# Kernel optimization log

Hardware: AMD Instinct MI355X
Metric: run time of the kernel (lower is better)

The kernel has to match this reference:

```python
import jax, jax.numpy as jnp
import numpy as np

B, L, D = 2, 2048, 1024
NUM_HEADS = 16
HEAD_DIM = D // NUM_HEADS


def setup_inputs() -> dict:
    key = jax.random.key(0)
    k1, k2 = jax.random.split(key)
    x = jax.random.normal(k1, (B, L, D), dtype=jnp.float32)
    # torch Linear(input_dim, 3*output_dim, bias=False); store as [in, 3*out] for x @ W
    W_qkv = jax.random.normal(k2, (D, 3 * D), dtype=jnp.float32) * (1.0 / np.sqrt(D))
    return {"x": x, "W_qkv": W_qkv}


def reference(x, W_qkv):
    b, l, d = x.shape
    h, hd = NUM_HEADS, HEAD_DIM
    qkv = x @ W_qkv                                  # [B, L, 3*D]
    qkv = qkv.reshape(b, l, 3, h, hd)
    q = jnp.transpose(qkv[:, :, 0], (0, 2, 1, 3))    # [B, H, L, hd]
    k = jnp.transpose(qkv[:, :, 1], (0, 2, 1, 3))
    v = jnp.transpose(qkv[:, :, 2], (0, 2, 1, 3))
    scale = 1.0 / jnp.sqrt(jnp.asarray(hd, dtype=x.dtype))
    scores = jnp.einsum('bhqd,bhkd->bhqk', q, k) * scale   # [B, H, L, L]
    causal = jnp.triu(jnp.ones((l, l), dtype=bool), k=1)   # True above diagonal -> masked
    scores = jnp.where(causal, -jnp.inf, scores)
    attn = jax.nn.softmax(scores, axis=-1)
    # dropout p=0.0 -> identity (eval mode)
    out = jnp.einsum('bhqk,bhkd->bhqd', attn, v)            # [B, H, L, hd]
    out = jnp.transpose(out, (0, 2, 1, 3)).reshape(b, l, h * hd)
    return out
```

## Files before the change

### kernel.cpp

```cpp
#include <hip/hip_runtime.h>
#include <hip/hip_bf16.h>
#include <math.h>

#define NB_L 2048
#define GM 4096
#define GN 3072
#define GK 1024
#define NROWS 65536
#define SCALE_L2E 0.180336880f

typedef float  f4v __attribute__((ext_vector_type(4)));
typedef short  s4v __attribute__((ext_vector_type(4)));
typedef short  s8v __attribute__((ext_vector_type(8)));

#define MFMA_16x16x32(a, b, c) __builtin_amdgcn_mfma_f32_16x16x32_bf16((a), (b), (c), 0, 0, 0)
#define MFMA_16x16x16(a, b, c) __builtin_amdgcn_mfma_f32_16x16x16bf16_1k((a), (b), (c), 0, 0, 0)

static __device__ __forceinline__ unsigned int bfpk(float a, float b) {
    __hip_bfloat162 h = __float22bfloat162_rn(float2{a, b});
    union { __hip_bfloat162 h2; unsigned int u; } cv; cv.h2 = h; return cv.u;
}
static __device__ __forceinline__ unsigned short bf1(float a) {
    union { __hip_bfloat16 h; unsigned short u; } cv; cv.h = __float2bfloat16(a); return cv.u;
}
static __device__ __forceinline__ float bf2f(unsigned short u) {
    union { unsigned int u; float f; } cv; cv.u = ((unsigned int)u) << 16; return cv.f;
}

static __device__ __forceinline__ void gl_lds16(const ushort* g, ushort* l) {
    __builtin_amdgcn_global_load_lds((const __attribute__((address_space(1))) void*)g,
                                     (__attribute__((address_space(3))) void*)l, 16, 0, 0);
}

__global__ __launch_bounds__(256) void conv_fused(
    const float* __restrict__ X, const float* __restrict__ W,
    ushort* __restrict__ Xb, ushort* __restrict__ Wt)
{
    __shared__ __align__(16) ushort T[64][72];
    const int bid = blockIdx.x, t = threadIdx.x;
    if (bid < 2048) {
        const int i = bid * 256 + t;
        const float4 f0 = ((const float4*)X)[2 * i];
        const float4 f1 = ((const float4*)X)[2 * i + 1];
        uint4 u;
        u.x = bfpk(f0.x, f0.y); u.y = bfpk(f0.z, f0.w);
        u.z = bfpk(f1.x, f1.y); u.w = bfpk(f1.z, f1.w);
        ((uint4*)Xb)[i] = u;
    } else {
        const int wb = bid - 2048;
        const int k0 = (wb & 15) * 64, n0 = (wb >> 4) * 64;
        {
            const int kr = t >> 2, nc0 = (t & 3) * 16;
            const float* src = W + (size_t)(k0 + kr) * GN + n0 + nc0;
#pragma unroll
            for (int u = 0; u < 4; ++u) {
                const float4 v = *(const float4*)(src + 4 * u);
                T[nc0 + 4 * u + 0][kr] = bf1(v.x);
                T[nc0 + 4 * u + 1][kr] = bf1(v.y);
                T[nc0 + 4 * u + 2][kr] = bf1(v.z);
                T[nc0 + 4 * u + 3][kr] = bf1(v.w);
            }
        }
        __syncthreads();
        {
            const int nr = t >> 2, kc0 = (t & 3) * 16;
            ushort* dst = Wt + (size_t)(n0 + nr) * GK + k0 + kc0;
            *(s8v*)dst       = *(const s8v*)&T[nr][kc0];
            *(s8v*)(dst + 8) = *(const s8v*)&T[nr][kc0 + 8];
        }
    }
}

__global__ __launch_bounds__(256, 2) void qkv_gemm_bf16(
    const ushort* __restrict__ Xb, const ushort* __restrict__ Wt,
    ushort* __restrict__ Qh, ushort* __restrict__ Kh, ushort* __restrict__ VT)
{
    __shared__ __align__(16) ushort As[2][2][128][32];
    __shared__ __align__(16) ushort Bs[2][2][192][32];

    const int tid = threadIdx.x;
    const int bid = blockIdx.x;

    const int xcd = bid & 7, idx = bid >> 3;
    const int ytile = ((xcd >> 1) << 3) + (idx & 7);
    const int xtile = ((xcd & 1) << 3) + (idx >> 3);
    const int row0 = ytile << 7;
    const int col0 = xtile * 192;

    const int lane = tid & 63, wn = tid >> 6;
    const int lq = lane & 15, quad = lane >> 4;

    const int rS = tid >> 2, pA = tid & 3;
    const int cA = pA ^ ((rS >> 1) & 3);
    const ushort* gA0 = Xb + (size_t)(row0 + rS) * GK + cA * 8;
    const ushort* gB0 = Wt + (size_t)(col0 + rS) * GK + cA * 8;

    const int pq = (quad ^ ((lq >> 1) & 3)) * 8;
    const int rowB = wn * 48;

    f4v acc[8][3];
#pragma unroll
    for (int mf = 0; mf < 8; ++mf)
#pragma unroll
        for (int nf = 0; nf < 3; ++nf) acc[mf][nf] = 0.f;

    auto stA = [&](int t, int h, int u) {
        gl_lds16(gA0 + (size_t)u * 64 * GK + t * 64 + h * 32,
                 &As[t & 1][h][u * 64 + rS][pA * 8]);
    };
    auto stB = [&](int t, int h, int u) {
        gl_lds16(gB0 + (size_t)u * 64 * GK + t * 64 + h * 32,
                 &Bs[t & 1][h][u * 64 + rS][pA * 8]);
    };

    stA(0, 0, 0); stA(0, 0, 1);
    stB(0, 0, 0); stB(0, 0, 1); stB(0, 0, 2);
    stA(0, 1, 0); stA(0, 1, 1);
    stB(0, 1, 0); stB(0, 1, 1); stB(0, 1, 2);
    stA(1, 0, 0); stA(1, 0, 1);
    stB(1, 0, 0); stB(1, 0, 1); stB(1, 0, 2);
    asm volatile("s_waitcnt vmcnt(5)" ::: "memory");
    __builtin_amdgcn_s_barrier();
    asm volatile("" ::: "memory");

    const int NT = GK / 64;
#pragma unroll 2
    for (int t = 0; t < NT; ++t) {
        const int cur = t & 1;
        s8v af[4], bfr[3];

#pragma unroll
        for (int nf = 0; nf < 3; ++nf) bfr[nf] = *(const s8v*)&Bs[cur][0][rowB + nf * 16 + lq][pq];
#pragma unroll
        for (int mf = 0; mf < 4; ++mf) af[mf] = *(const s8v*)&As[cur][0][mf * 16 + lq][pq];
        if (t + 1 < NT) { stB(t + 1, 1, 0); stB(t + 1, 1, 1); stB(t + 1, 1, 2); }
        __builtin_amdgcn_s_barrier();
        asm volatile("s_waitcnt lgkmcnt(0)");
        __builtin_amdgcn_s_setprio(1);
#pragma unroll
        for (int mf = 0; mf < 4; ++mf)
#pragma unroll
            for (int nf = 0; nf < 3; ++nf)
                acc[mf][nf] = MFMA_16x16x32(af[mf], bfr[nf], acc[mf][nf]);
        __builtin_amdgcn_s_setprio(0);
        __builtin_amdgcn_s_barrier();

#pragma unroll
        for (int mf = 0; mf < 4; ++mf) af[mf] = *(const s8v*)&As[cur][0][64 + mf * 16 + lq][pq];
        if (t + 1 < NT) { stA(t + 1, 1, 0); stA(t + 1, 1, 1); }
        __builtin_amdgcn_s_barrier();
        asm volatile("s_waitcnt lgkmcnt(0)");
        __builtin_amdgcn_s_setprio(1);
#pragma unroll
        for (int mf = 0; mf < 4; ++mf)
#pragma unroll
            for (int nf = 0; nf < 3; ++nf)
                acc[mf + 4][nf] = MFMA_16x16x32(af[mf], bfr[nf], acc[mf + 4][nf]);
        __builtin_amdgcn_s_setprio(0);
        __builtin_amdgcn_s_barrier();

#pragma unroll
        for (int nf = 0; nf < 3; ++nf) bfr[nf] = *(const s8v*)&Bs[cur][1][rowB + nf * 16 + lq][pq];
#pragma unroll
        for (int mf = 0; mf < 4; ++mf) af[mf] = *(const s8v*)&As[cur][1][mf * 16 + lq][pq];
        if (t + 2 < NT) { stA(t + 2, 0, 0); stA(t + 2, 0, 1); }
        __builtin_amdgcn_s_barrier();
        asm volatile("s_waitcnt lgkmcnt(0)");
        __builtin_amdgcn_s_setprio(1);
#pragma unroll
        for (int mf = 0; mf < 4; ++mf)
#pragma unroll
            for (int nf = 0; nf < 3; ++nf)
                acc[mf][nf] = MFMA_16x16x32(af[mf], bfr[nf], acc[mf][nf]);
        __builtin_amdgcn_s_setprio(0);
        __builtin_amdgcn_s_barrier();

#pragma unroll
        for (int mf = 0; mf < 4; ++mf) af[mf] = *(const s8v*)&As[cur][1][64 + mf * 16 + lq][pq];
        if (t + 2 < NT) { stB(t + 2, 0, 0); stB(t + 2, 0, 1); stB(t + 2, 0, 2); }
        __builtin_amdgcn_s_barrier();
        asm volatile("s_waitcnt lgkmcnt(0)");
        __builtin_amdgcn_s_setprio(1);
#pragma unroll
        for (int mf = 0; mf < 4; ++mf)
#pragma unroll
            for (int nf = 0; nf < 3; ++nf)
                acc[mf + 4][nf] = MFMA_16x16x32(af[mf], bfr[nf], acc[mf + 4][nf]);
        __builtin_amdgcn_s_setprio(0);
        if (t + 2 < NT) asm volatile("s_waitcnt vmcnt(5)" ::: "memory");
        else            asm volatile("s_waitcnt vmcnt(0)" ::: "memory");
        __builtin_amdgcn_s_barrier();
        asm volatile("" ::: "memory");
    }

#pragma unroll
    for (int mf = 0; mf < 8; ++mf)
#pragma unroll
        for (int nf = 0; nf < 3; ++nf) {
            const int colg = col0 + wn * 48 + nf * 16 + lq;
            const int part = colg >> 10;
            const int colp = colg & 1023;
            const int hh = colp >> 6, d = colp & 63;
#pragma unroll
            for (int r = 0; r < 4; ++r) {
                const int row = row0 + mf * 16 + quad * 4 + r;
                const int b = row >> 11, tok = row & 2047;
                const int bh = b * 16 + hh;
                if (part == 0) {
                    Qh[((size_t)bh * 2048 + tok) * 64 + d] = bf1(acc[mf][nf][r] * SCALE_L2E);
                } else if (part == 1) {
                    Kh[((size_t)bh * 2048 + tok) * 64 + (d ^ ((tok & 7) << 3))] = bf1(acc[mf][nf][r]);
                } else {
                    VT[((size_t)bh * 64 + d) * 2048 + (tok ^ ((d & 7) << 3))] = bf1(acc[mf][nf][r]);
                }
            }
        }
}

__global__ __launch_bounds__(256, 4) void attn_bf16(
    const ushort* __restrict__ Qh, const ushort* __restrict__ Kh,
    const ushort* __restrict__ VT, ushort* __restrict__ Opart, float* __restrict__ Lp)
{
    __shared__ __align__(16) ushort Ks[2][64 * 64];
    __shared__ __align__(16) ushort Vt[2][64 * 64];

    const int x = blockIdx.x;
    const int bh = x & 31;
    const int qlow = (x >> 5) & 7;
    const int s = (x >> 8) & 1;
    const int x9 = (x >> 9) & 1;
    const int qt = x9 ? (15 - qlow) : qlow;

    const int tid = threadIdx.x;
    const int w = tid >> 6, lane = tid & 63;
    const int lq = lane & 15, quad = lane >> 4;
    const int kswz = (lq & 7) << 3;
    const int qrow_base = qt * 128 + w * 32;
    const int diag = 2 * qt + (w >> 1);

    s8v qf[2][2];
#pragma unroll
    for (int qg = 0; qg < 2; ++qg)
#pragma unroll
        for (int sb = 0; sb < 2; ++sb)
            qf[qg][sb] = *(const s8v*)(Qh + ((size_t)bh * 2048 + qrow_base + qg * 16 + lq) * 64
                                       + sb * 32 + quad * 8);

    f4v o[4][2];
#pragma unroll
    for (int dg = 0; dg < 4; ++dg)
#pragma unroll
        for (int qg = 0; qg < 2; ++qg) o[dg][qg] = 0.f;
    f4v lacc[2]; lacc[0] = 0.f; lacc[1] = 0.f;
    const s4v ones = { (short)0x3F80, (short)0x3F80, (short)0x3F80, (short)0x3F80 };

    const int kt_lo = s ? (qt + 1) : 0;
    const int kt_hi = s ? (2 * qt + 1) : qt;
    const int niter = kt_hi - kt_lo + 1;

    const ushort* kbase = Kh + (size_t)bh * 2048 * 64;
    const ushort* vbase = VT + (size_t)bh * 64 * 2048;
    const int g1 = tid, g2 = tid + 256;
    const int kr1 = g1 >> 3, ko1 = (g1 & 7) * 8;
    const int kr2 = g2 >> 3, ko2 = (g2 & 7) * 8;

    auto stage = [&](int kt, int bufi) {
        const ushort* kt_k = kbase + (size_t)kt * 64 * 64;
        const ushort* kt_v = vbase + kt * 64;
        gl_lds16(kt_k + kr1 * 64 + ko1,           &Ks[bufi][g1 * 8]);
        gl_lds16(kt_k + kr2 * 64 + ko2,           &Ks[bufi][g2 * 8]);
        gl_lds16(kt_v + (size_t)kr1 * 2048 + ko1, &Vt[bufi][g1 * 8]);
        gl_lds16(kt_v + (size_t)kr2 * 2048 + ko2, &Vt[bufi][g2 * 8]);
    };

    auto compute = [&](int ktc, int bufi) {
        if (ktc > diag) return;
        f4v st[4][2];
#pragma unroll
        for (int kg = 0; kg < 4; ++kg)
#pragma unroll
            for (int qg = 0; qg < 2; ++qg) st[kg][qg] = 0.f;
#pragma unroll
        for (int kg = 0; kg < 4; ++kg)
#pragma unroll
            for (int sb = 0; sb < 2; ++sb) {
                const s8v af = *(const s8v*)&Ks[bufi][(kg * 16 + lq) * 64
                                                     + ((sb * 32 + quad * 8) ^ kswz)];
#pragma unroll
                for (int qg = 0; qg < 2; ++qg)
                    st[kg][qg] = MFMA_16x16x32(af, qf[qg][sb], st[kg][qg]);
            }
        if (ktc == diag) {
#pragma unroll
            for (int kg = 0; kg < 4; ++kg)
#pragma unroll
                for (int qg = 0; qg < 2; ++qg) {
                    const int qrow = qrow_base + qg * 16 + lq;
#pragma unroll
                    for (int r = 0; r < 4; ++r)
                        if (ktc * 64 + kg * 16 + quad * 4 + r > qrow)
                            st[kg][qg][r] = -INFINITY;
                }
        }
#pragma unroll
        for (int kg = 0; kg < 4; ++kg)
#pragma unroll
            for (int qg = 0; qg < 2; ++qg)
#pragma unroll
                for (int r = 0; r < 4; ++r)
                    st[kg][qg][r] = exp2f(st[kg][qg][r]);
#pragma unroll
        for (int ks = 0; ks < 4; ++ks) {
            s4v pb[2];
#pragma unroll
            for (int qg = 0; qg < 2; ++qg) {
                union { s4v v; uint2 u; } c;
                c.u.x = bfpk(st[ks][qg][0], st[ks][qg][1]);
                c.u.y = bfpk(st[ks][qg][2], st[ks][qg][3]);
                pb[qg] = c.v;
            }
#pragma unroll
            for (int qg = 0; qg < 2; ++qg)
                lacc[qg] = MFMA_16x16x16(ones, pb[qg], lacc[qg]);
#pragma unroll
            for (int dg = 0; dg < 4; ++dg) {
                const s4v va = *(const s4v*)&Vt[bufi][(dg * 16 + lq) * 64
                                                     + ((ks * 16 + quad * 4) ^ kswz)];
#pragma unroll
                for (int qg = 0; qg < 2; ++qg)
                    o[dg][qg] = MFMA_16x16x16(va, pb[qg], o[dg][qg]);
            }
        }
    };

    stage(kt_lo, 0);
    for (int i = 0; i < niter; ++i) {
        const int cur = i & 1;
        __syncthreads();
        if (i + 1 < niter) stage(kt_lo + i + 1, cur ^ 1);
        compute(kt_lo + i, cur);
    }

#pragma unroll
    for (int qg = 0; qg < 2; ++qg) {
        const size_t prow = (size_t)(s * 32 + bh) * 2048 + qrow_base + qg * 16 + lq;
#pragma unroll
        for (int dg = 0; dg < 4; ++dg) {
            const int d = dg * 16 + quad * 4;
            uint2 u;
            u.x = bfpk(o[dg][qg][0], o[dg][qg][1]);
            u.y = bfpk(o[dg][qg][2], o[dg][qg][3]);
            *(uint2*)&Opart[prow * 64 + d] = u;
        }
        if (quad == 0) Lp[prow] = lacc[qg][0];
    }
}

__global__ __launch_bounds__(256) void attn_combine(
    const ushort* __restrict__ Opart, const float* __restrict__ Lp, float* __restrict__ Out)
{
    const int id = blockIdx.x * 256 + threadIdx.x;
    const int row = id >> 4, c4 = (id & 15) * 4;
    const float l0 = Lp[row], l1 = Lp[row + NROWS];
    const float inv = 1.0f / (l0 + l1);

    const s4v a = *(const s4v*)&Opart[(size_t)row * 64 + c4];
    const s4v c = *(const s4v*)&Opart[(size_t)(row + NROWS) * 64 + c4];
    float4 v;
    v.x = (bf2f((unsigned short)a[0]) + bf2f((unsigned short)c[0])) * inv;
    v.y = (bf2f((unsigned short)a[1]) + bf2f((unsigned short)c[1])) * inv;
    v.z = (bf2f((unsigned short)a[2]) + bf2f((unsigned short)c[2])) * inv;
    v.w = (bf2f((unsigned short)a[3]) + bf2f((unsigned short)c[3])) * inv;

    const int bh = row >> 11, qrow = row & 2047;
    const int b = bh >> 4, h = bh & 15;
    *(float4*)(Out + ((size_t)(b * 2048 + qrow)) * 1024 + h * 64 + c4) = v;
}

extern "C" void kernel_launch(void* const* d_in, const int* in_sizes, int n_in,
                              void* d_out, int out_size, void* d_ws, size_t ws_size,
                              hipStream_t stream)
{
    const float* x  = (const float*)d_in[0];
    const float* wq = (const float*)d_in[1];
    float* out = (float*)d_out;

    const size_t HEADTEN = (size_t)32 * 2048 * 64;
    ushort* wsp = (ushort*)d_ws;
    ushort* qh = wsp;
    ushort* kh = qh + HEADTEN;
    ushort* vt = kh + HEADTEN;
    ushort* xb = vt + HEADTEN;
    ushort* wt = xb + (size_t)GM * GK;
    ushort* opart = xb;
    float*  lp    = (float*)(opart + (size_t)2 * NROWS * 64);

    conv_fused<<<2816, 256, 0, stream>>>(x, wq, xb, wt);
    qkv_gemm_bf16<<<512, 256, 0, stream>>>(xb, wt, qh, kh, vt);
    attn_bf16<<<1024, 256, 0, stream>>>(qh, kh, vt, opart, lp);
    attn_combine<<<NROWS * 16 / 256, 256, 0, stream>>>(opart, lp, out);
}
```

Before: 171.3 us.

## Enlarge QKV GEMM tile to 128x384 with 8 waves in a 2x4 grid

The QKV projection GEMM now uses 512-thread blocks, each computing a 128x384 output tile. The eight waves sit in a 2x4 grid, each owning a 64x96 sub-tile, in place of four waves each covering 128x48. Each block loads fewer A rows per B column, which raises operand reuse per LDS byte, and the grid shrinks to 256 blocks. The cost is more LDS per block (larger B buffer), possibly lower occupancy, and fewer blocks, which may underfill the 256 CUs.

Result: no change. 172.7 us (+0.8%).

```diff
diff --git a/kernel.cpp b/kernel.cpp
--- a/kernel.cpp
+++ b/kernel.cpp
@@ -71,23 +71,24 @@
     }
 }
 
-__global__ __launch_bounds__(256, 2) void qkv_gemm_bf16(
+__global__ __launch_bounds__(512, 2) void qkv_gemm_bf16(
     const ushort* __restrict__ Xb, const ushort* __restrict__ Wt,
     ushort* __restrict__ Qh, ushort* __restrict__ Kh, ushort* __restrict__ VT)
 {
     __shared__ __align__(16) ushort As[2][2][128][32];
-    __shared__ __align__(16) ushort Bs[2][2][192][32];
+    __shared__ __align__(16) ushort Bs[2][2][384][32];
 
     const int tid = threadIdx.x;
     const int bid = blockIdx.x;
 
     const int xcd = bid & 7, idx = bid >> 3;
     const int ytile = ((xcd >> 1) << 3) + (idx & 7);
-    const int xtile = ((xcd & 1) << 3) + (idx >> 3);
+    const int xtile = ((xcd & 1) << 2) + (idx >> 3);
     const int row0 = ytile << 7;
-    const int col0 = xtile * 192;
-
-    const int lane = tid & 63, wn = tid >> 6;
+    const int col0 = xtile * 384;
+
+    const int lane = tid & 63, w = tid >> 6;
+    const int wm = w >> 2, wn = w & 3;
     const int lq = lane & 15, quad = lane >> 4;
 
     const int rS = tid >> 2, pA = tid & 3;
@@ -96,30 +97,30 @@
     const ushort* gB0 = Wt + (size_t)(col0 + rS) * GK + cA * 8;
 
     const int pq = (quad ^ ((lq >> 1) & 3)) * 8;
-    const int rowB = wn * 48;
-
-    f4v acc[8][3];
-#pragma unroll
-    for (int mf = 0; mf < 8; ++mf)
-#pragma unroll
-        for (int nf = 0; nf < 3; ++nf) acc[mf][nf] = 0.f;
-
-    auto stA = [&](int t, int h, int u) {
-        gl_lds16(gA0 + (size_t)u * 64 * GK + t * 64 + h * 32,
-                 &As[t & 1][h][u * 64 + rS][pA * 8]);
+    const int rowA = wm * 64 + lq;
+    const int rowB = wn * 96 + lq;
+
+    f4v acc[4][6];
+#pragma unroll
+    for (int mf = 0; mf < 4; ++mf)
+#pragma unroll
+        for (int nf = 0; nf < 6; ++nf) acc[mf][nf] = 0.f;
+
+    auto stA = [&](int t, int h) {
+        gl_lds16(gA0 + t * 64 + h * 32, &As[t & 1][h][rS][pA * 8]);
     };
     auto stB = [&](int t, int h, int u) {
-        gl_lds16(gB0 + (size_t)u * 64 * GK + t * 64 + h * 32,
-                 &Bs[t & 1][h][u * 64 + rS][pA * 8]);
+        gl_lds16(gB0 + (size_t)u * 128 * GK + t * 64 + h * 32,
+                 &Bs[t & 1][h][u * 128 + rS][pA * 8]);
     };
 
-    stA(0, 0, 0); stA(0, 0, 1);
+    stA(0, 0);
     stB(0, 0, 0); stB(0, 0, 1); stB(0, 0, 2);
-    stA(0, 1, 0); stA(0, 1, 1);
+    stA(0, 1);
     stB(0, 1, 0); stB(0, 1, 1); stB(0, 1, 2);
-    stA(1, 0, 0); stA(1, 0, 1);
+    stA(1, 0);
     stB(1, 0, 0); stB(1, 0, 1); stB(1, 0, 2);
-    asm volatile("s_waitcnt vmcnt(5)" ::: "memory");
+    asm volatile("s_waitcnt vmcnt(4)" ::: "memory");
     __builtin_amdgcn_s_barrier();
     asm volatile("" ::: "memory");
 
@@ -130,9 +131,9 @@
         s8v af[4], bfr[3];
 
 #pragma unroll
-        for (int nf = 0; nf < 3; ++nf) bfr[nf] = *(const s8v*)&Bs[cur][0][rowB + nf * 16 + lq][pq];
-#pragma unroll
-        for (int mf = 0; mf < 4; ++mf) af[mf] = *(const s8v*)&As[cur][0][mf * 16 + lq][pq];
+        for (int nf = 0; nf < 3; ++nf) bfr[nf] = *(const s8v*)&Bs[cur][0][rowB + nf * 16][pq];
+#pragma unroll
+        for (int mf = 0; mf < 4; ++mf) af[mf] = *(const s8v*)&As[cur][0][rowA + mf * 16][pq];
         if (t + 1 < NT) { stB(t + 1, 1, 0); stB(t + 1, 1, 1); stB(t + 1, 1, 2); }
         __builtin_amdgcn_s_barrier();
         asm volatile("s_waitcnt lgkmcnt(0)");
@@ -146,8 +147,8 @@
         __builtin_amdgcn_s_barrier();
 
 #pragma unroll
-        for (int mf = 0; mf < 4; ++mf) af[mf] = *(const s8v*)&As[cur][0][64 + mf * 16 + lq][pq];
-        if (t + 1 < NT) { stA(t + 1, 1, 0); stA(t + 1, 1, 1); }
+        for (int nf = 0; nf < 3; ++nf) bfr[nf] = *(const s8v*)&Bs[cur][0][rowB + 48 + nf * 16][pq];
+        if (t + 1 < NT) stA(t + 1, 1);
         __builtin_amdgcn_s_barrier();
         asm volatile("s_waitcnt lgkmcnt(0)");
         __builtin_amdgcn_s_setprio(1);
@@ -155,15 +156,15 @@
         for (int mf = 0; mf < 4; ++mf)
 #pragma unroll
             for (int nf = 0; nf < 3; ++nf)
-                acc[mf + 4][nf] = MFMA_16x16x32(af[mf], bfr[nf], acc[mf + 4][nf]);
+                acc[mf][nf + 3] = MFMA_16x16x32(af[mf], bfr[nf], acc[mf][nf + 3]);
         __builtin_amdgcn_s_setprio(0);
         __builtin_amdgcn_s_barrier();
 
 #pragma unroll
-        for (int nf = 0; nf < 3; ++nf) bfr[nf] = *(const s8v*)&Bs[cur][1][rowB + nf * 16 + lq][pq];
-#pragma unroll
-        for (int mf = 0; mf < 4; ++mf) af[mf] = *(const s8v*)&As[cur][1][mf * 16 + lq][pq];
-        if (t + 2 < NT) { stA(t + 2, 0, 0); stA(t + 2, 0, 1); }
+        for (int nf = 0; nf < 3; ++nf) bfr[nf] = *(const s8v*)&Bs[cur][1][rowB + nf * 16][pq];
+#pragma unroll
+        for (int mf = 0; mf < 4; ++mf) af[mf] = *(const s8v*)&As[cur][1][rowA + mf * 16][pq];
+        if (t + 2 < NT) stA(t + 2, 0);
         __builtin_amdgcn_s_barrier();
         asm volatile("s_waitcnt lgkmcnt(0)");
         __builtin_amdgcn_s_setprio(1);
@@ -176,7 +177,7 @@
         __builtin_amdgcn_s_barrier();
 
 #pragma unroll
-        for (int mf = 0; mf < 4; ++mf) af[mf] = *(const s8v*)&As[cur][1][64 + mf * 16 + lq][pq];
+        for (int nf = 0; nf < 3; ++nf) bfr[nf] = *(const s8v*)&Bs[cur][1][rowB + 48 + nf * 16][pq];
         if (t + 2 < NT) { stB(t + 2, 0, 0); stB(t + 2, 0, 1); stB(t + 2, 0, 2); }
         __builtin_amdgcn_s_barrier();
         asm volatile("s_waitcnt lgkmcnt(0)");
@@ -185,25 +186,25 @@
         for (int mf = 0; mf < 4; ++mf)
 #pragma unroll
             for (int nf = 0; nf < 3; ++nf)
-                acc[mf + 4][nf] = MFMA_16x16x32(af[mf], bfr[nf], acc[mf + 4][nf]);
+                acc[mf][nf + 3] = MFMA_16x16x32(af[mf], bfr[nf], acc[mf][nf + 3]);
         __builtin_amdgcn_s_setprio(0);
-        if (t + 2 < NT) asm volatile("s_waitcnt vmcnt(5)" ::: "memory");
+        if (t + 2 < NT) asm volatile("s_waitcnt vmcnt(4)" ::: "memory");
         else            asm volatile("s_waitcnt vmcnt(0)" ::: "memory");
         __builtin_amdgcn_s_barrier();
         asm volatile("" ::: "memory");
     }
 
 #pragma unroll
-    for (int mf = 0; mf < 8; ++mf)
-#pragma unroll
-        for (int nf = 0; nf < 3; ++nf) {
-            const int colg = col0 + wn * 48 + nf * 16 + lq;
+    for (int mf = 0; mf < 4; ++mf)
+#pragma unroll
+        for (int nf = 0; nf < 6; ++nf) {
+            const int colg = col0 + wn * 96 + nf * 16 + lq;
             const int part = colg >> 10;
             const int colp = colg & 1023;
             const int hh = colp >> 6, d = colp & 63;
 #pragma unroll
             for (int r = 0; r < 4; ++r) {
-                const int row = row0 + mf * 16 + quad * 4 + r;
+                const int row = row0 + wm * 64 + mf * 16 + quad * 4 + r;
                 const int b = row >> 11, tok = row & 2047;
                 const int bh = b * 16 + hh;
                 if (part == 0) {
@@ -396,7 +397,7 @@
     float*  lp    = (float*)(opart + (size_t)2 * NROWS * 64);
 
     conv_fused<<<2816, 256, 0, stream>>>(x, wq, xb, wt);
-    qkv_gemm_bf16<<<512, 256, 0, stream>>>(xb, wt, qh, kh, vt);
+    qkv_gemm_bf16<<<256, 512, 0, stream>>>(xb, wt, qh, kh, vt);
     attn_bf16<<<1024, 256, 0, stream>>>(qh, kh, vt, opart, lp);
     attn_combine<<<NROWS * 16 / 256, 256, 0, stream>>>(opart, lp, out);
 }
```
